# Performance work log

Hardware: AMD Instinct MI355X
Metric: run time of the kernel (lower is better)

## Reference

```python
import jax, jax.numpy as jnp
import numpy as np

IN_CH, HID, OUT_CH, HEADS = 55, 128, 49, 4
D = HID * HEADS  # 512
N_NODES, N_EDGES = 20000, 320000
NEG_SLOPE = 0.2


def setup_inputs() -> dict:
    key = jax.random.key(0)
    ks = jax.random.split(key, 16)
    s = lambda *sh: 1.0 / np.sqrt(sh[0])
    x = jax.random.normal(ks[0], (N_NODES, IN_CH), dtype=jnp.float32)
    edge_index = jax.random.randint(ks[1], (2, N_EDGES), 0, N_NODES, dtype=jnp.int64)
    p = {
        'x': x,
        'edge_index': edge_index,
        # conv1 (GATv2: lin_l for source, lin_r for target, per-head att vector, out bias)
        'w1_l': jax.random.normal(ks[2], (IN_CH, D), jnp.float32) * s(IN_CH),
        'b1_l': jnp.zeros((D,), jnp.float32),
        'w1_r': jax.random.normal(ks[3], (IN_CH, D), jnp.float32) * s(IN_CH),
        'b1_r': jnp.zeros((D,), jnp.float32),
        'att1': jax.random.normal(ks[4], (HEADS, HID), jnp.float32) * s(HID),
        'bias1': jnp.zeros((D,), jnp.float32),
        # conv2
        'w2_l': jax.random.normal(ks[5], (D, D), jnp.float32) * s(D),
        'b2_l': jnp.zeros((D,), jnp.float32),
        'w2_r': jax.random.normal(ks[6], (D, D), jnp.float32) * s(D),
        'b2_r': jnp.zeros((D,), jnp.float32),
        'att2': jax.random.normal(ks[7], (HEADS, HID), jnp.float32) * s(HID),
        'bias2': jnp.zeros((D,), jnp.float32),
        # classifier
        'w_cls': jax.random.normal(ks[8], (D, OUT_CH), jnp.float32) * s(D),
        'b_cls': jnp.zeros((OUT_CH,), jnp.float32),
    }
    return p


def _gatv2(x, src, dst, n, wl, bl, wr, br, att, bias):
    # GATv2Conv, concat=True. messages flow src -> dst, softmax over dst neighborhoods.
    xl = (x @ wl + bl).reshape(n, HEADS, HID)  # source transform
    xr = (x @ wr + br).reshape(n, HEADS, HID)  # target transform
    e = jax.nn.leaky_relu(xl[src] + xr[dst], NEG_SLOPE)      # [E, H, C]
    score = jnp.einsum('ehc,hc->eh', e, att)                  # [E, H]
    m = jax.ops.segment_max(score, dst, num_segments=n)       # stable softmax per target
    alpha = jnp.exp(score - m[dst])
    denom = jax.ops.segment_sum(alpha, dst, num_segments=n)
    alpha = alpha / denom[dst]
    out = jax.ops.segment_sum(xl[src] * alpha[..., None], dst, num_segments=n)
    return out.reshape(n, D) + bias


def reference(x, edge_index, w1_l, b1_l, w1_r, b1_r, att1, bias1,
              w2_l, b2_l, w2_r, b2_r, att2, bias2, w_cls, b_cls):
    n = x.shape[0]
    # PyG GATv2Conv default add_self_loops=True
    loops = jnp.arange(n, dtype=edge_index.dtype)
    src = jnp.concatenate([edge_index[0], loops])
    dst = jnp.concatenate([edge_index[1], loops])
    h = _gatv2(x, src, dst, n, w1_l, b1_l, w1_r, b1_r, att1, bias1)
    h = jax.nn.elu(h)
    # dropout p=0.5 is identity at eval time
    h = _gatv2(h, src, dst, n, w2_l, b2_l, w2_r, b2_r, att2, bias2)
    h = jax.nn.elu(h)
    return h @ w_cls + b_cls
```

## Files before the change

### kernel.cpp

```cpp
#include <hip/hip_runtime.h>
#include <hip/hip_bf16.h>
#include <float.h>
#include <math.h>

#define N_NODES 20000
#define N_EDGES 320000
#define ET      (N_EDGES + N_NODES)
#define ETB     ((ET + 255) / 256)
#define NPB     ((N_NODES + 255) / 256)
#define DCH     512
#define D2      1024
#define INCH    55
#define INCHP   64
#define OUTCH   49
#define OUTCHP  128
#define NB      130

typedef _Float16 f16;
typedef _Float16 f16x2 __attribute__((ext_vector_type(2)));
typedef _Float16 f16x8 __attribute__((ext_vector_type(8)));
typedef float    f32x4 __attribute__((ext_vector_type(4)));

#define GPTR(p) ((const __attribute__((address_space(1))) void*)(p))
#define LPTR(p) ((__attribute__((address_space(3))) void*)(p))

__device__ __forceinline__ void transpose_tile(const float* __restrict__ w, f16* __restrict__ o,
                                               int K, int N, int Kp, int bx, int by, int t,
                                               f16 (*tile)[66]) {
    int k0 = by * 64, n0 = bx * 64;
    #pragma unroll
    for (int r = 0; r < 16; ++r) {
        int kl = (t >> 6) + r * 4, nl = t & 63;
        int gk = k0 + kl, gn = n0 + nl;
        tile[kl][nl] = (gk < K && gn < N) ? (f16)w[(size_t)gk * N + gn] : (f16)0.f;
    }
    __syncthreads();
    #pragma unroll
    for (int r = 0; r < 16; ++r) {
        int kl = t & 63, nl = (t >> 6) + r * 4;
        o[(size_t)(n0 + nl) * Kp + k0 + kl] = tile[kl][nl];
    }
}

__global__ __launch_bounds__(256) void prep_all(const float* __restrict__ x, f16* __restrict__ x_h,
                                                const float* __restrict__ w1l, const float* __restrict__ w1r,
                                                const float* __restrict__ w2l, const float* __restrict__ w2r,
                                                const float* __restrict__ wc,
                                                f16* __restrict__ w1T, f16* __restrict__ w2T,
                                                f16* __restrict__ wcT,
                                                int* __restrict__ zeroA,
                                                int* __restrict__ bcur) {
    __shared__ f16 tile[64][66];
    int b = blockIdx.x, t = threadIdx.x;
    if (b < 157) {
        int i = b * 256 + t;
        if (i < 40000) zeroA[i] = 0;
        else if (i < 40000 + NB) bcur[i - 40000] = 0;
        return;
    }
    b -= 157;
    if (b < 5000) {
        int i = b * 256 + t;
        int r = i >> 6, c = i & 63;
        x_h[i] = (c < INCH) ? (f16)x[r * INCH + c] : (f16)0.f;
        return;
    }
    b -= 5000;
    if (b < 8)  { transpose_tile(w1l, w1T, INCH, DCH, INCHP, b, 0, t, tile); return; }
    b -= 8;
    if (b < 8)  { transpose_tile(w1r, w1T + (size_t)DCH * INCHP, INCH, DCH, INCHP, b, 0, t, tile); return; }
    b -= 8;
    if (b < 64) { transpose_tile(w2l, w2T, DCH, DCH, DCH, b & 7, b >> 3, t, tile); return; }
    b -= 64;
    if (b < 64) { transpose_tile(w2r, w2T + (size_t)DCH * DCH, DCH, DCH, DCH, b & 7, b >> 3, t, tile); return; }
    b -= 64;
    transpose_tile(wc, wcT, DCH, OUTCH, DCH, b & 1, b >> 1, t, tile);
}

__global__ void count_kernel(const int* __restrict__ ei, int* __restrict__ counts) {
    int e = blockIdx.x * blockDim.x + threadIdx.x;
    if (e >= ET) return;
    int d = (e < N_EDGES) ? ei[N_EDGES + e] : (e - N_EDGES);
    atomicAdd(&counts[d], 1);
}

__global__ void scan_kernel(const int* __restrict__ counts, int* __restrict__ row_ptr,
                            int* __restrict__ bbase) {
    __shared__ int sdata[1024];
    __shared__ int bh[NB];
    int t = threadIdx.x;
    if (t < NB) bh[t] = 0;
    __syncthreads();
    int per = (N_NODES + 1023) / 1024;
    int b = t * per, e = min(N_NODES, b + per);
    int sum = 0;
    for (int i = b; i < e; ++i) {
        int c = counts[i];
        sum += c;
        atomicAdd(&bh[min(c, NB - 1)], 1);
    }
    sdata[t] = sum;
    __syncthreads();
    for (int off = 1; off < 1024; off <<= 1) {
        int v = (t >= off) ? sdata[t - off] : 0;
        __syncthreads();
        sdata[t] += v;
        __syncthreads();
    }
    int run = (t == 0) ? 0 : sdata[t - 1];
    if (t == 0) row_ptr[0] = 0;
    for (int i = b; i < e; ++i) { run += counts[i]; row_ptr[i + 1] = run; }
    __syncthreads();
    if (t == 0) {
        int acc = 0;
        for (int j = NB - 1; j >= 0; --j) { bbase[j] = acc; acc += bh[j]; }
    }
}

__global__ __launch_bounds__(256) void fill_perm_kernel(const int* __restrict__ ei,
                                                        const int* __restrict__ row_ptr,
                                                        const int* __restrict__ counts,
                                                        const int* __restrict__ bbase,
                                                        int* __restrict__ cursor,
                                                        int* __restrict__ bcur,
                                                        int* __restrict__ esrc,
                                                        int* __restrict__ perm) {
    int blk = blockIdx.x;
    if (blk < ETB) {
        int e = blk * 256 + threadIdx.x;
        if (e >= ET) return;
        int s, d;
        if (e < N_EDGES) { s = ei[e]; d = ei[N_EDGES + e]; }
        else             { s = d = e - N_EDGES; }
        int pos = row_ptr[d] + atomicAdd(&cursor[d], 1);
        esrc[pos] = s;
        return;
    }
    blk -= ETB;
    __shared__ int hist[NB], basep[NB];
    int t = threadIdx.x;
    for (int i = t; i < NB; i += 256) hist[i] = 0;
    __syncthreads();
    int n = blk * 256 + t;
    bool valid = n < N_NODES;
    int bkt = 0, rl = 0;
    if (valid) {
        bkt = min(counts[n], NB - 1);
        rl = atomicAdd(&hist[bkt], 1);
    }
    __syncthreads();
    for (int i = t; i < NB; i += 256)
        if (hist[i] > 0) basep[i] = atomicAdd(&bcur[i], hist[i]);
    __syncthreads();
    if (valid) perm[bbase[bkt] + basep[bkt] + rl] = n;
}

template<int OUT_F16, int DUAL>
__global__ __launch_bounds__(256) void gemm_f16(const f16* __restrict__ A,
                                                const f16* __restrict__ BT,
                                                const float* __restrict__ bl,
                                                const float* __restrict__ br,
                                                void* __restrict__ Cout,
                                                int M, int Ka, int Nv, int ldc) {
    __shared__ __align__(16) f16 As[128][64];
    __shared__ __align__(16) f16 Bs[128][64];
    const int tid = threadIdx.x;
    const int w = tid >> 6, lane = tid & 63;
    int nbx = gridDim.x;
    int nwg = nbx * gridDim.y;
    int bid = blockIdx.y * nbx + blockIdx.x;
    if ((nwg & 7) == 0) bid = (bid & 7) * (nwg >> 3) + (bid >> 3);
    const int m0 = (bid / nbx) * 128, n0 = (bid % nbx) * 128;
    const int wr = (w >> 1) * 64, wc = (w & 1) * 64;
    const int lrow = lane & 15, lk = lane >> 4;
    const int sw = lrow & 7;

    f32x4 acc[4][4] = {};

    for (int k0 = 0; k0 < Ka; k0 += 64) {
        #pragma unroll
        for (int i = 0; i < 4; ++i) {
            int idx = tid + 256 * i;
            int row = idx >> 3;
            int cg  = (idx & 7) ^ (row & 7);
            int gm = m0 + row; gm = gm < M ? gm : M - 1;
            const f16* gp = A + (size_t)gm * Ka + k0 + cg * 8;
            f16* lp = &As[0][0] + (size_t)(w * 64 + 256 * i) * 8;
            __builtin_amdgcn_global_load_lds(GPTR(gp), LPTR(lp), 16, 0, 0);
        }
        #pragma unroll
        for (int i = 0; i < 4; ++i) {
            int idx = tid + 256 * i;
            int row = idx >> 3;
            int cg  = (idx & 7) ^ (row & 7);
            const f16* gp = BT + (size_t)(n0 + row) * Ka + k0 + cg * 8;
            f16* lp = &Bs[0][0] + (size_t)(w * 64 + 256 * i) * 8;
            __builtin_amdgcn_global_load_lds(GPTR(gp), LPTR(lp), 16, 0, 0);
        }
        __syncthreads();
        #pragma unroll
        for (int kk = 0; kk < 64; kk += 32) {
            f16x8 af[4], bf[4];
            #pragma unroll
            for (int m = 0; m < 4; ++m)
                af[m] = *(const f16x8*)&As[wr + m * 16 + lrow][(((kk >> 3) + lk) ^ sw) * 8];
            #pragma unroll
            for (int n = 0; n < 4; ++n)
                bf[n] = *(const f16x8*)&Bs[wc + n * 16 + lrow][(((kk >> 3) + lk) ^ sw) * 8];
            #pragma unroll
            for (int m = 0; m < 4; ++m)
                #pragma unroll
                for (int n = 0; n < 4; ++n)
                    acc[m][n] = __builtin_amdgcn_mfma_f32_16x16x32_f16(af[m], bf[n], acc[m][n], 0, 0, 0);
        }
        __syncthreads();
    }

    const int orow = (lane >> 4) * 4, ocol = lane & 15;
    #pragma unroll
    for (int m = 0; m < 4; ++m) {
        #pragma unroll
        for (int r = 0; r < 4; ++r) {
            int gm = m0 + wr + m * 16 + orow + r;
            if (gm >= M) continue;
            #pragma unroll
            for (int n = 0; n < 4; ++n) {
                int gn = n0 + wc + n * 16 + ocol;
                if (gn >= Nv) continue;
                float bv = DUAL ? (gn < DCH ? bl[gn] : br[gn - DCH]) : bl[gn];
                float v = acc[m][n][r] + bv;
                if (OUT_F16) ((f16*)Cout)[(size_t)gm * ldc + gn] = (f16)v;
                else         ((float*)Cout)[(size_t)gm * ldc + gn] = v;
            }
        }
    }
}

#define PROC(cc0, cc1, pp)                                                      \
  {                                                                             \
    float sc0 = 0.f, sc1 = 0.f;                                                 \
    _Pragma("unroll")                                                           \
    for (int j = 0; j < 4; ++j) {                                               \
        f16x2 u0 = cc0.q[j] + xr0.q[j];                                         \
        f16x2 u1 = cc1.q[j] + xr1.q[j];                                         \
        f16x2 l0 = __builtin_elementwise_max(u0, u0 * k02);                     \
        f16x2 l1 = __builtin_elementwise_max(u1, u1 * k02);                     \
        sc0 = __builtin_amdgcn_fdot2(l0, at2[j], sc0, false);                   \
        sc1 = __builtin_amdgcn_fdot2(l1, at2[j], sc1, false);                   \
    }                                                                           \
    _Pragma("unroll")                                                           \
    for (int o = 8; o >= 1; o >>= 1) {                                          \
        sc0 += __shfl_xor(sc0, o, 64);                                          \
        sc1 += __shfl_xor(sc1, o, 64);                                          \
    }                                                                           \
    if ((pp) >= deg0) sc0 = -INFINITY;                                          \
    if ((pp) >= deg1) sc1 = -INFINITY;                                          \
    if (__any(sc0 > m0 + 8.f)) {                                                \
        float mn = fmaxf(m0, sc0); float f = __expf(m0 - mn);                   \
        d0 *= f;                                                                \
        _Pragma("unroll") for (int j = 0; j < 8; ++j) acc0[j] *= f;             \
        m0 = mn;                                                                \
    }                                                                           \
    float w0 = __expf(sc0 - m0); d0 += w0;                                      \
    _Pragma("unroll") for (int j = 0; j < 8; ++j) acc0[j] += w0 * (float)cc0.v[j]; \
    if (__any(sc1 > m1 + 8.f)) {                                                \
        float mn = fmaxf(m1, sc1); float f = __expf(m1 - mn);                   \
        d1 *= f;                                                                \
        _Pragma("unroll") for (int j = 0; j < 8; ++j) acc1[j] *= f;             \
        m1 = mn;                                                                \
    }                                                                           \
    float w1 = __expf(sc1 - m1); d1 += w1;                                      \
    _Pragma("unroll") for (int j = 0; j < 8; ++j) acc1[j] += w1 * (float)cc1.v[j]; \
  }

__global__ __launch_bounds__(256) void edge_agg6(const int* __restrict__ row_ptr,
                                                 const int* __restrict__ esrc,
                                                 const int* __restrict__ perm,
                                                 const f16* __restrict__ xlr,
                                                 const float* __restrict__ att,
                                                 const float* __restrict__ bias,
                                                 f16* __restrict__ out) {
    int wv = (blockIdx.x * 256 + threadIdx.x) >> 6;
    if (wv * 2 >= N_NODES) return;
    int n0 = perm[wv * 2], n1 = perm[wv * 2 + 1];
    int lane = threadIdx.x & 63;

    union U8 { f16x8 v; f16x2 q[4]; };
    U8 xr0, xr1;
    xr0.v = *(const f16x8*)(xlr + (size_t)n0 * D2 + DCH + lane * 8);
    xr1.v = *(const f16x8*)(xlr + (size_t)n1 * D2 + DCH + lane * 8);
    const float4* av = (const float4*)(att + lane * 8);
    float4 a0 = av[0], a1 = av[1];
    f16x2 at2[4] = { f16x2{(f16)a0.x, (f16)a0.y}, f16x2{(f16)a0.z, (f16)a0.w},
                     f16x2{(f16)a1.x, (f16)a1.y}, f16x2{(f16)a1.z, (f16)a1.w} };
    const f16x2 k02 = {(f16)0.2f, (f16)0.2f};

    int beg0 = row_ptr[n0], deg0 = row_ptr[n0 + 1] - beg0;
    int beg1 = row_ptr[n1], deg1 = row_ptr[n1 + 1] - beg1;
    int pre0 = (lane < deg0) ? esrc[beg0 + lane] : 0;
    int pre1 = (lane < deg1) ? esrc[beg1 + lane] : 0;

    float acc0[8] = {}, acc1[8] = {};
    float m0 = -FLT_MAX, m1 = -FLT_MAX, d0 = 0.f, d1 = 0.f;

    int dmax = deg0 > deg1 ? deg0 : deg1;
    int dcap = dmax < 64 ? dmax : 64;

    U8 cA0, cA1, cB0, cB1;
    {
        int s0 = __shfl(pre0, 0, 64), s1 = __shfl(pre1, 0, 64);
        cA0.v = *(const f16x8*)(xlr + (size_t)s0 * D2 + lane * 8);
        cA1.v = *(const f16x8*)(xlr + (size_t)s1 * D2 + lane * 8);
    }
    int p = 0;
    for (; p + 1 < dcap; p += 2) {
        int t0 = __shfl(pre0, p + 1, 64), t1 = __shfl(pre1, p + 1, 64);
        cB0.v = *(const f16x8*)(xlr + (size_t)t0 * D2 + lane * 8);
        cB1.v = *(const f16x8*)(xlr + (size_t)t1 * D2 + lane * 8);
        PROC(cA0, cA1, p)
        if (p + 2 < dcap) {
            int u0 = __shfl(pre0, p + 2, 64), u1 = __shfl(pre1, p + 2, 64);
            cA0.v = *(const f16x8*)(xlr + (size_t)u0 * D2 + lane * 8);
            cA1.v = *(const f16x8*)(xlr + (size_t)u1 * D2 + lane * 8);
        }
        PROC(cB0, cB1, p + 1)
    }
    if (p < dcap) PROC(cA0, cA1, p)
    for (p = 64; p < dmax; ++p) {
        int s0 = (p < deg0) ? esrc[beg0 + p] : -1;
        int s1 = (p < deg1) ? esrc[beg1 + p] : -1;
        U8 t0, t1;
        t0.v = *(const f16x8*)(xlr + (size_t)(s0 < 0 ? 0 : s0) * D2 + lane * 8);
        t1.v = *(const f16x8*)(xlr + (size_t)(s1 < 0 ? 0 : s1) * D2 + lane * 8);
        PROC(t0, t1, p)
    }

    const float4* bv = (const float4*)(bias + lane * 8);
    float4 b0 = bv[0], b1 = bv[1];
    float bf[8] = {b0.x, b0.y, b0.z, b0.w, b1.x, b1.y, b1.z, b1.w};
    float i0 = 1.f / d0, i1 = 1.f / d1;
    f16x8 o0, o1;
    #pragma unroll
    for (int j = 0; j < 8; ++j) {
        float v0 = acc0[j] * i0 + bf[j];
        float v1 = acc1[j] * i1 + bf[j];
        v0 = v0 > 0.f ? v0 : __expf(v0) - 1.f;
        v1 = v1 > 0.f ? v1 : __expf(v1) - 1.f;
        o0[j] = (f16)v0;
        o1[j] = (f16)v1;
    }
    *(f16x8*)(out + (size_t)n0 * DCH + lane * 8) = o0;
    *(f16x8*)(out + (size_t)n1 * DCH + lane * 8) = o1;
}

extern "C" void kernel_launch(void* const* d_in, const int* in_sizes, int n_in,
                              void* d_out, int out_size, void* d_ws, size_t ws_size,
                              hipStream_t stream) {
    const float* x     = (const float*)d_in[0];
    const int*   ei    = (const int*)d_in[1];
    const float* w1_l  = (const float*)d_in[2];
    const float* b1_l  = (const float*)d_in[3];
    const float* w1_r  = (const float*)d_in[4];
    const float* b1_r  = (const float*)d_in[5];
    const float* att1  = (const float*)d_in[6];
    const float* bias1 = (const float*)d_in[7];
    const float* w2_l  = (const float*)d_in[8];
    const float* b2_l  = (const float*)d_in[9];
    const float* w2_r  = (const float*)d_in[10];
    const float* b2_r  = (const float*)d_in[11];
    const float* att2  = (const float*)d_in[12];
    const float* bias2 = (const float*)d_in[13];
    const float* wcls  = (const float*)d_in[14];
    const float* bcls  = (const float*)d_in[15];
    float* out = (float*)d_out;

    char* ws = (char*)d_ws;
    f16* x_h = (f16*)ws;
    f16* w1T = x_h + (size_t)N_NODES * INCHP;
    f16* w2T = w1T + (size_t)D2 * INCHP;
    f16* wcT = w2T + (size_t)D2 * DCH;
    f16* xlr = wcT + (size_t)OUTCHP * DCH;
    f16* h   = xlr + (size_t)N_NODES * D2;
    int* row_ptr = (int*)(h + (size_t)N_NODES * DCH);
    int* counts  = row_ptr + (N_NODES + 1);
    int* cursor  = counts + N_NODES;
    int* esrc    = cursor + N_NODES;
    int* perm    = esrc + ET;
    int* bbase   = perm + N_NODES;
    int* bcur    = bbase + NB;

    prep_all<<<5317, 256, 0, stream>>>(x, x_h, w1_l, w1_r, w2_l, w2_r, wcls,
                                       w1T, w2T, wcT, counts, bcur);
    count_kernel<<<(ET + 255) / 256, 256, 0, stream>>>(ei, counts);
    scan_kernel<<<1, 1024, 0, stream>>>(counts, row_ptr, bbase);
    fill_perm_kernel<<<ETB + NPB, 256, 0, stream>>>(ei, row_ptr, counts, bbase,
                                                    cursor, bcur, esrc, perm);

    dim3 blk(256);
    dim3 gD(D2 / 128, (N_NODES + 127) / 128);
    dim3 gC(1, (N_NODES + 127) / 128);
    int eb = (N_NODES / 2 + 3) / 4;

    gemm_f16<1, 1><<<gD, blk, 0, stream>>>(x_h, w1T, b1_l, b1_r, xlr, N_NODES, INCHP, D2, D2);
    edge_agg6<<<eb, blk, 0, stream>>>(row_ptr, esrc, perm, xlr, att1, bias1, h);
    gemm_f16<1, 1><<<gD, blk, 0, stream>>>(h, w2T, b2_l, b2_r, xlr, N_NODES, DCH, D2, D2);
    edge_agg6<<<eb, blk, 0, stream>>>(row_ptr, esrc, perm, xlr, att2, bias2, h);
    gemm_f16<0, 0><<<gC, blk, 0, stream>>>(h, wcT, bcls, bcls, out, N_NODES, DCH, OUTCH, OUTCH);
}
```

Measured before the change: 273.7 us.

## Double-buffer GEMM K-tiles and deepen edge gather prefetch to three stages

```diff
diff --git a/kernel.cpp b/kernel.cpp
--- a/kernel.cpp
+++ b/kernel.cpp
@@ -162,8 +162,8 @@
                                                 const float* __restrict__ br,
                                                 void* __restrict__ Cout,
                                                 int M, int Ka, int Nv, int ldc) {
-    __shared__ __align__(16) f16 As[128][64];
-    __shared__ __align__(16) f16 Bs[128][64];
+    __shared__ __align__(16) f16 As[2][128][32];
+    __shared__ __align__(16) f16 Bs[2][128][32];
     const int tid = threadIdx.x;
     const int w = tid >> 6, lane = tid & 63;
     int nbx = gridDim.x;
@@ -173,48 +173,54 @@
     const int m0 = (bid / nbx) * 128, n0 = (bid % nbx) * 128;
     const int wr = (w >> 1) * 64, wc = (w & 1) * 64;
     const int lrow = lane & 15, lk = lane >> 4;
-    const int sw = lrow & 7;
+    const int gr = lk ^ ((lrow >> 1) & 3);
 
     f32x4 acc[4][4] = {};
 
-    for (int k0 = 0; k0 < Ka; k0 += 64) {
+#define STAGE(BUF, KK0)                                                         \
+    {                                                                           \
+        _Pragma("unroll")                                                       \
+        for (int i = 0; i < 4; ++i) {                                           \
+            int idx = tid + 256 * i;                                            \
+            int g   = idx & 511;                                                \
+            int row = g >> 2;                                                   \
+            int cgs = (g & 3) ^ ((row >> 1) & 3);                               \
+            const f16* gp;                                                      \
+            f16* lp;                                                            \
+            if (i < 2) {                                                        \
+                int gm = m0 + row; gm = gm < M ? gm : M - 1;                    \
+                gp = A + (size_t)gm * Ka + (KK0) + cgs * 8;                     \
+                lp = &As[BUF][0][0] + (w * 64 + (i & 1) * 256) * 8;             \
+            } else {                                                            \
+                gp = BT + (size_t)(n0 + row) * Ka + (KK0) + cgs * 8;            \
+                lp = &Bs[BUF][0][0] + (w * 64 + (i & 1) * 256) * 8;             \
+            }                                                                   \
+            __builtin_amdgcn_global_load_lds(GPTR(gp), LPTR(lp), 16, 0, 0);     \
+        }                                                                       \
+    }
+
+    const int nt = Ka >> 5;
+    STAGE(0, 0)
+    __syncthreads();
+    int cur = 0;
+    for (int t = 0; t < nt; ++t) {
+        if (t + 1 < nt) STAGE(cur ^ 1, (t + 1) * 32)
+        f16x8 af[4], bf[4];
         #pragma unroll
-        for (int i = 0; i < 4; ++i) {
-            int idx = tid + 256 * i;
-            int row = idx >> 3;
-            int cg  = (idx & 7) ^ (row & 7);
-            int gm = m0 + row; gm = gm < M ? gm : M - 1;
-            const f16* gp = A + (size_t)gm * Ka + k0 + cg * 8;
-            f16* lp = &As[0][0] + (size_t)(w * 64 + 256 * i) * 8;
-            __builtin_amdgcn_global_load_lds(GPTR(gp), LPTR(lp), 16, 0, 0);
-        }
+        for (int m = 0; m < 4; ++m)
+            af[m] = *(const f16x8*)&As[cur][wr + m * 16 + lrow][gr * 8];
         #pragma unroll
-        for (int i = 0; i < 4; ++i) {
-            int idx = tid + 256 * i;
-            int row = idx >> 3;
-            int cg  = (idx & 7) ^ (row & 7);
-            const f16* gp = BT + (size_t)(n0 + row) * Ka + k0 + cg * 8;
-            f16* lp = &Bs[0][0] + (size_t)(w * 64 + 256 * i) * 8;
-            __builtin_amdgcn_global_load_lds(GPTR(gp), LPTR(lp), 16, 0, 0);
-        }
-        __syncthreads();
+        for (int n = 0; n < 4; ++n)
+            bf[n] = *(const f16x8*)&Bs[cur][wc + n * 16 + lrow][gr * 8];
         #pragma unroll
-        for (int kk = 0; kk < 64; kk += 32) {
-            f16x8 af[4], bf[4];
-            #pragma unroll
-            for (int m = 0; m < 4; ++m)
-                af[m] = *(const f16x8*)&As[wr + m * 16 + lrow][(((kk >> 3) + lk) ^ sw) * 8];
+        for (int m = 0; m < 4; ++m)
             #pragma unroll
             for (int n = 0; n < 4; ++n)
-                bf[n] = *(const f16x8*)&Bs[wc + n * 16 + lrow][(((kk >> 3) + lk) ^ sw) * 8];
-            #pragma unroll
-            for (int m = 0; m < 4; ++m)
-                #pragma unroll
-                for (int n = 0; n < 4; ++n)
-                    acc[m][n] = __builtin_amdgcn_mfma_f32_16x16x32_f16(af[m], bf[n], acc[m][n], 0, 0, 0);
-        }
+                acc[m][n] = __builtin_amdgcn_mfma_f32_16x16x32_f16(af[m], bf[n], acc[m][n], 0, 0, 0);
         __syncthreads();
-    }
+        cur ^= 1;
+    }
+#undef STAGE
 
     const int orow = (lane >> 4) * 4, ocol = lane & 15;
     #pragma unroll
@@ -273,7 +279,15 @@
     _Pragma("unroll") for (int j = 0; j < 8; ++j) acc1[j] += w1 * (float)cc1.v[j]; \
   }
 
-__global__ __launch_bounds__(256) void edge_agg6(const int* __restrict__ row_ptr,
+#define LOADU(B0, B1, pp)                                                       \
+  {                                                                             \
+    int q = (pp) < dcap ? (pp) : dcap - 1;                                      \
+    int s0 = __shfl(pre0, q, 64), s1 = __shfl(pre1, q, 64);                     \
+    B0.v = *(const f16x8*)(xlr + (size_t)s0 * D2 + lane * 8);                   \
+    B1.v = *(const f16x8*)(xlr + (size_t)s1 * D2 + lane * 8);                   \
+  }
+
+__global__ __launch_bounds__(256) void edge_agg7(const int* __restrict__ row_ptr,
                                                  const int* __restrict__ esrc,
                                                  const int* __restrict__ perm,
                                                  const f16* __restrict__ xlr,
@@ -306,32 +320,25 @@
     int dmax = deg0 > deg1 ? deg0 : deg1;
     int dcap = dmax < 64 ? dmax : 64;
 
-    U8 cA0, cA1, cB0, cB1;
-    {
-        int s0 = __shfl(pre0, 0, 64), s1 = __shfl(pre1, 0, 64);
-        cA0.v = *(const f16x8*)(xlr + (size_t)s0 * D2 + lane * 8);
-        cA1.v = *(const f16x8*)(xlr + (size_t)s1 * D2 + lane * 8);
-    }
-    int p = 0;
-    for (; p + 1 < dcap; p += 2) {
-        int t0 = __shfl(pre0, p + 1, 64), t1 = __shfl(pre1, p + 1, 64);
-        cB0.v = *(const f16x8*)(xlr + (size_t)t0 * D2 + lane * 8);
-        cB1.v = *(const f16x8*)(xlr + (size_t)t1 * D2 + lane * 8);
+    U8 cA0, cA1, cB0, cB1, cC0, cC1;
+    LOADU(cA0, cA1, 0)
+    LOADU(cB0, cB1, 1)
+    for (int p = 0; p < dcap; p += 3) {
+        LOADU(cC0, cC1, p + 2)
         PROC(cA0, cA1, p)
-        if (p + 2 < dcap) {
-            int u0 = __shfl(pre0, p + 2, 64), u1 = __shfl(pre1, p + 2, 64);
-            cA0.v = *(const f16x8*)(xlr + (size_t)u0 * D2 + lane * 8);
-            cA1.v = *(const f16x8*)(xlr + (size_t)u1 * D2 + lane * 8);
-        }
+        if (p + 1 >= dcap) break;
+        LOADU(cA0, cA1, p + 3)
         PROC(cB0, cB1, p + 1)
-    }
-    if (p < dcap) PROC(cA0, cA1, p)
-    for (p = 64; p < dmax; ++p) {
-        int s0 = (p < deg0) ? esrc[beg0 + p] : -1;
-        int s1 = (p < deg1) ? esrc[beg1 + p] : -1;
+        if (p + 2 >= dcap) break;
+        LOADU(cB0, cB1, p + 4)
+        PROC(cC0, cC1, p + 2)
+    }
+    for (int p = 64; p < dmax; ++p) {
+        int s0 = (p < deg0) ? esrc[beg0 + p] : 0;
+        int s1 = (p < deg1) ? esrc[beg1 + p] : 0;
         U8 t0, t1;
-        t0.v = *(const f16x8*)(xlr + (size_t)(s0 < 0 ? 0 : s0) * D2 + lane * 8);
-        t1.v = *(const f16x8*)(xlr + (size_t)(s1 < 0 ? 0 : s1) * D2 + lane * 8);
+        t0.v = *(const f16x8*)(xlr + (size_t)s0 * D2 + lane * 8);
+        t1.v = *(const f16x8*)(xlr + (size_t)s1 * D2 + lane * 8);
         PROC(t0, t1, p)
     }
 
@@ -402,8 +409,8 @@
     int eb = (N_NODES / 2 + 3) / 4;
 
     gemm_f16<1, 1><<<gD, blk, 0, stream>>>(x_h, w1T, b1_l, b1_r, xlr, N_NODES, INCHP, D2, D2);
-    edge_agg6<<<eb, blk, 0, stream>>>(row_ptr, esrc, perm, xlr, att1, bias1, h);
+    edge_agg7<<<eb, blk, 0, stream>>>(row_ptr, esrc, perm, xlr, att1, bias1, h);
     gemm_f16<1, 1><<<gD, blk, 0, stream>>>(h, w2T, b2_l, b2_r, xlr, N_NODES, DCH, D2, D2);
-    edge_agg6<<<eb, blk, 0, stream>>>(row_ptr, esrc, perm, xlr, att2, bias2, h);
+    edge_agg7<<<eb, blk, 0, stream>>>(row_ptr, esrc, perm, xlr, att2, bias2, h);
     gemm_f16<0, 0><<<gC, blk, 0, stream>>>(h, wcT, bcls, bcls, out, N_NODES, DCH, OUTCH, OUTCH);
 }
```

Measured after the change: 275.5 us. Within noise of the previous version (+0.6%).
